# Kernel optimization log

Measured on AMD Instinct MI355X. Metric: run time of the kernel, lower is better.

Reference implementation:

```python
import jax, jax.numpy as jnp
import numpy as np

N = 50000   # nodes
E = 800000  # edges
C = 64      # node feature channels (0e)
A = 4       # edge attr channels
B = 16      # edge embedding (radial basis) size
H = 8       # radial MLP hidden size
D = 32      # query/key channels
P = 16      # node attr channels
R_MAX = 5.0


def setup_inputs() -> dict:
    key = jax.random.key(0)
    ks = jax.random.split(key, 20)
    w = lambda k, shape, fan_in: (jax.random.normal(k, shape, jnp.float32) / np.sqrt(fan_in).astype(np.float32))
    inp = {
        "node_feats": jax.random.normal(ks[0], (N, C), jnp.float32),
        "node_attrs": jax.random.normal(ks[1], (N, P), jnp.float32),
        "edge_embedding": jax.random.uniform(ks[2], (E, B), jnp.float32),
        "edge_attrs": jax.random.normal(ks[3], (E, A), jnp.float32),
        "positions": jax.random.normal(ks[4], (N, 3), jnp.float32) * 0.3,  # keep lengths < r_max
        "edge_src": jax.random.randint(ks[5], (E,), 0, N),
        "edge_dst": jax.random.randint(ks[6], (E,), 0, N),
        # parameters
        "W_q": w(ks[7], (C, D), C),            # h_q Linear
        "W1_k": w(ks[8], (B, H), B),           # radial MLP for tp_k
        "W2_k": w(ks[9], (H, C * A), H),
        "W1_v": w(ks[10], (B, H), B),          # radial MLP for tp_v
        "W2_v": w(ks[11], (H, C * A), H),
        "W_lin_k": w(ks[12], (C, D), C),       # linear_k
        "W_lin_v": w(ks[13], (C, C), C),       # linear_v
        "W_dot": w(ks[14], (D, D), D * D),     # FullyConnectedTensorProduct(q,k,'0e')
        "W_sc": w(ks[15], (C, P, C), C * P),   # self connection FCTP
    }
    return inp


def soft_unit_step(x):
    safe = jnp.where(x > 0, x, 1.0)
    return jnp.where(x > 0, jnp.exp(-1.0 / safe), 0.0)


def uvu_tp(x_src, edge_attrs, edge_embedding, W1, W2):
    # radial MLP -> per-edge, per-path weights [E, C, A]; 'uvu' tensor product on scalars
    wgt = (jax.nn.silu(edge_embedding @ W1) @ W2).reshape(-1, C, A)
    return x_src * (jnp.einsum('eca,ea->ec', wgt, edge_attrs) / np.sqrt(A).astype(np.float32))


def reference(node_feats, node_attrs, edge_embedding, edge_attrs, positions,
              edge_src, edge_dst, W_q, W1_k, W2_k, W1_v, W2_v,
              W_lin_k, W_lin_v, W_dot, W_sc):
    q = (node_feats @ W_q)[edge_dst]                              # [E, D]
    x_src = node_feats[edge_src]                                  # [E, C]
    k = uvu_tp(x_src, edge_attrs, edge_embedding, W1_k, W2_k) @ W_lin_k  # [E, D]
    v = uvu_tp(x_src, edge_attrs, edge_embedding, W1_v, W2_v) @ W_lin_v  # [E, C]

    edge_vec = positions[edge_dst] - positions[edge_src]
    edge_length = jnp.linalg.norm(edge_vec, axis=1)               # [E]
    cutoff = soft_unit_step(2.0 * R_MAX * (1.0 - edge_length / R_MAX))

    score = jnp.einsum('ei,ij,ej->e', q, W_dot, k)                # weighted bilinear dot -> 0e
    expv = cutoff * jnp.exp(score)                                # [E]
    z = jax.ops.segment_sum(expv, edge_dst, num_segments=N)       # softmax normalizer
    z = jnp.where(z == 0, 1.0, z)
    alpha = expv / z[edge_dst]
    msg = jnp.sqrt(jax.nn.relu(alpha))[:, None] * v               # [E, C]
    node_out = jax.ops.segment_sum(msg, edge_dst, num_segments=N)  # [N, C]

    sc = jnp.einsum('nc,np,cpo->no', node_feats, node_attrs, W_sc)
    return node_out + sc
```

## Files before the change

### kernel.cpp

```cpp
#include <hip/hip_runtime.h>
#include <math.h>

#define NN 50000
#define EE 800000
#define NPAD 50176
#define CPAD 68

typedef __attribute__((ext_vector_type(8))) short short8v;
typedef __attribute__((ext_vector_type(4))) float f32x4;

static __device__ __forceinline__ short bf16r(float x) {
  union { float f; unsigned u; } v; v.f = x;
  unsigned r = v.u + 0x7FFFu + ((v.u >> 16) & 1u);
  return (short)(r >> 16);
}
static __device__ __forceinline__ float bf2f(unsigned u) {
  union { unsigned u; float f; } v; v.u = u << 16;
  return v.f;
}
static __device__ __forceinline__ unsigned pk2(float a, float b) {
  return (unsigned)(unsigned short)bf16r(a) | ((unsigned)(unsigned short)bf16r(b) << 16);
}


__global__ __launch_bounds__(256) void fold_kernel(
    const float* __restrict__ Wq, const float* __restrict__ Wdot,
    const float* __restrict__ Wlk, const float* __restrict__ W2k,
    const float* __restrict__ W2v, const float* __restrict__ Wlv,
    float* __restrict__ M, unsigned short* __restrict__ w2kT,
    unsigned short* __restrict__ w2vT, unsigned short* __restrict__ wlvb)
{
  __shared__ float tmp[2048];
  const int tid = threadIdx.x;
#pragma unroll
  for (int r = 0; r < 8; ++r) {
    int idx = tid + r * 256;
    int cin = idx >> 5, d = idx & 31;
    float a = 0.f;
    for (int j = 0; j < 32; ++j) a = fmaf(Wq[cin * 32 + j], Wdot[j * 32 + d], a);
    tmp[idx] = a;
  }
  __syncthreads();
#pragma unroll
  for (int r = 0; r < 16; ++r) {
    int idx = tid + r * 256;
    int cin = idx >> 6, c = idx & 63;
    float a = 0.f;
    for (int d = 0; d < 32; ++d) a = fmaf(tmp[cin * 32 + d], Wlk[c * 32 + d], a);
    M[idx] = a;
  }
#pragma unroll
  for (int r = 0; r < 8; ++r) {
    int idx = tid + r * 256;
    int c = idx >> 5, k = idx & 31, h = k >> 2, a = k & 3;
    w2kT[idx] = (unsigned short)bf16r(W2k[h * 256 + c * 4 + a]);
    w2vT[idx] = (unsigned short)bf16r(W2v[h * 256 + c * 4 + a]);
  }
#pragma unroll
  for (int r = 0; r < 16; ++r) {
    int idx = tid + r * 256;
    int o = idx >> 6, c = idx & 63;
    wlvb[idx] = (unsigned short)bf16r(Wlv[c * 64 + o]);
  }
}

__global__ __launch_bounds__(256) void prep_wsc(
    const float* __restrict__ Wsc, unsigned short* __restrict__ wscb)
{
  int w = blockIdx.x * 256 + threadIdx.x;
  int c = w & 63, o = (w >> 6) & 63, p = w >> 12;
  wscb[w] = (unsigned short)bf16r(Wsc[c * 1024 + p * 64 + o]);
}

__global__ __launch_bounds__(256) void hist_kernel(
    const int* __restrict__ edst, int* __restrict__ cur)
{
  int e = blockIdx.x * 256 + threadIdx.x;
  atomicAdd(&cur[edst[e]], 1);
}

__global__ __launch_bounds__(256) void scanA_kernel(
    int* __restrict__ cur, int* __restrict__ bsum)
{
  __shared__ int s[256];
  const int tid = threadIdx.x;
  const int i = blockIdx.x * 256 + tid;
  int v = cur[i];
  s[tid] = v;
  __syncthreads();
  for (int off = 1; off < 256; off <<= 1) {
    int t = (tid >= off) ? s[tid - off] : 0;
    __syncthreads();
    s[tid] += t;
    __syncthreads();
  }
  cur[i] = s[tid] - v;
  if (tid == 255) bsum[blockIdx.x] = s[255];
}

__global__ __launch_bounds__(256) void scanB_kernel(int* __restrict__ bsum)
{
  __shared__ int s[256];
  const int tid = threadIdx.x;
  int v = (tid < 196) ? bsum[tid] : 0;
  s[tid] = v;
  __syncthreads();
  for (int off = 1; off < 256; off <<= 1) {
    int t = (tid >= off) ? s[tid - off] : 0;
    __syncthreads();
    s[tid] += t;
    __syncthreads();
  }
  if (tid < 196) bsum[tid] = s[tid] - v;
}

__global__ __launch_bounds__(256) void scanC_kernel(
    int* __restrict__ cur, const int* __restrict__ bsum)
{
  const int i = blockIdx.x * 256 + threadIdx.x;
  cur[i] += bsum[blockIdx.x];
}

__global__ __launch_bounds__(256) void scatter_fused(
    const int* __restrict__ esrc, const int* __restrict__ edst,
    const float* __restrict__ ea, const float* __restrict__ eb,
    const float* __restrict__ pos, const float* __restrict__ W1k,
    const float* __restrict__ W1v, int* __restrict__ cur,
    float* __restrict__ rec)
{
  int e = blockIdx.x * 256 + threadIdx.x;
  int s = esrc[e], d = edst[e];
  int r = atomicAdd(&cur[d], 1);
  float dx = pos[d * 3 + 0] - pos[s * 3 + 0];
  float dy = pos[d * 3 + 1] - pos[s * 3 + 1];
  float dz = pos[d * 3 + 2] - pos[s * 3 + 2];
  float len = sqrtf(fmaf(dx, dx, fmaf(dy, dy, dz * dz)));
  float arg = 10.f - 2.f * len;
  float cl = (arg > 0.f) ? __expf(-1.f / arg) : 0.f;
  const f32x4* eb4 = reinterpret_cast<const f32x4*>(eb);
  f32x4 q0 = eb4[e * 4 + 0], q1 = eb4[e * 4 + 1],
        q2 = eb4[e * 4 + 2], q3 = eb4[e * 4 + 3];
  float ebv[16] = {q0.x, q0.y, q0.z, q0.w, q1.x, q1.y, q1.z, q1.w,
                   q2.x, q2.y, q2.z, q2.w, q3.x, q3.y, q3.z, q3.w};
  float h[16];
#pragma unroll
  for (int j = 0; j < 16; ++j) h[j] = 0.f;
#pragma unroll
  for (int b = 0; b < 16; ++b) {
    float x = ebv[b];
#pragma unroll
    for (int j = 0; j < 8; ++j) {
      h[j]     = fmaf(x, W1k[b * 8 + j], h[j]);
      h[8 + j] = fmaf(x, W1v[b * 8 + j], h[8 + j]);
    }
  }
#pragma unroll
  for (int j = 0; j < 16; ++j) h[j] = h[j] / (1.f + __expf(-h[j]));

  f32x4* rp4 = reinterpret_cast<f32x4*>(rec + (size_t)r * 16);
  f32x4 w0, w1, w2, w3;
  w0.x = __int_as_float(s); w0.y = __int_as_float(d); w0.z = cl; w0.w = 0.f;
  w1 = reinterpret_cast<const f32x4*>(ea)[e];
  w2.x = __uint_as_float(pk2(h[0], h[1]));
  w2.y = __uint_as_float(pk2(h[2], h[3]));
  w2.z = __uint_as_float(pk2(h[4], h[5]));
  w2.w = __uint_as_float(pk2(h[6], h[7]));
  w3.x = __uint_as_float(pk2(h[8], h[9]));
  w3.y = __uint_as_float(pk2(h[10], h[11]));
  w3.z = __uint_as_float(pk2(h[12], h[13]));
  w3.w = __uint_as_float(pk2(h[14], h[15]));
  __builtin_nontemporal_store(w0, rp4 + 0);
  __builtin_nontemporal_store(w1, rp4 + 1);
  __builtin_nontemporal_store(w2, rp4 + 2);
  __builtin_nontemporal_store(w3, rp4 + 3);
}

__global__ __launch_bounds__(256) void tq_kernel(
    const float* __restrict__ nf, const float* __restrict__ M, float* __restrict__ tq)
{
  __shared__ float Ml[4096];
  __shared__ float nfl[64 * 68];
  const int tid = threadIdx.x;
  const int base = blockIdx.x * 64;
#pragma unroll
  for (int r = 0; r < 4; ++r) {
    int idx = tid + r * 256;
    reinterpret_cast<float4*>(Ml)[idx] = reinterpret_cast<const float4*>(M)[idx];
  }
#pragma unroll
  for (int r = 0; r < 4; ++r) {
    int idx = tid + r * 256;
    int row = idx >> 4, c4 = idx & 15;
    float4 v = make_float4(0.f, 0.f, 0.f, 0.f);
    if (base + row < NN) v = reinterpret_cast<const float4*>(nf)[(base + row) * 16 + c4];
    *reinterpret_cast<float4*>(&nfl[row * 68 + c4 * 4]) = v;
  }
  __syncthreads();
  const int to = tid & 15, tn = tid >> 4;
  float4 acc[4] = {make_float4(0,0,0,0), make_float4(0,0,0,0),
                   make_float4(0,0,0,0), make_float4(0,0,0,0)};
  for (int c = 0; c < 64; ++c) {
    float4 m = reinterpret_cast<const float4*>(Ml)[c * 16 + to];
#pragma unroll
    for (int i = 0; i < 4; ++i) {
      float x = nfl[(tn * 4 + i) * 68 + c];
      acc[i].x = fmaf(x, m.x, acc[i].x);
      acc[i].y = fmaf(x, m.y, acc[i].y);
      acc[i].z = fmaf(x, m.z, acc[i].z);
      acc[i].w = fmaf(x, m.w, acc[i].w);
    }
  }
#pragma unroll
  for (int i = 0; i < 4; ++i) {
    int n = base + tn * 4 + i;
    if (n < NN) reinterpret_cast<float4*>(tq)[n * 16 + to] = acc[i];
  }
}

__global__ __launch_bounds__(256) void edge_kernel(
    const float* __restrict__ nf, const float* __restrict__ tq,
    const float* __restrict__ rec,
    const unsigned short* __restrict__ w2kT, const unsigned short* __restrict__ w2vT,
    float* __restrict__ z, float* __restrict__ U)
{
  __shared__ float xs[64 * CPAD];
  __shared__ int   es[64];
  __shared__ int   ed[64];
  __shared__ float cl[64];
  __shared__ float evs[64];
  const int tid  = threadIdx.x;
  const int lane = tid & 63;
  const int lo = lane & 15, hi = lane >> 4;
  const int w = tid >> 6;
  const int sb = blockIdx.x * 64;
  const int row = 16 * w + lo;

  short8v bk[4], bv[4];
#pragma unroll
  for (int t = 0; t < 4; ++t) {
    bk[t] = *reinterpret_cast<const short8v*>(&w2kT[(16 * t + lo) * 32 + hi * 8]);
    bv[t] = *reinterpret_cast<const short8v*>(&w2vT[(16 * t + lo) * 32 + hi * 8]);
  }
  if (tid < 64) {
    float4 h0 = *reinterpret_cast<const float4*>(rec + (size_t)(sb + tid) * 16);
    es[tid] = __float_as_int(h0.x);
    ed[tid] = __float_as_int(h0.y);
    cl[tid] = h0.z;
  }
  const unsigned* ru = reinterpret_cast<const unsigned*>(rec);
  const size_t rb = (size_t)(sb + row) * 16;
  unsigned k01 = ru[rb + 8 + hi];
  unsigned v01 = ru[rb + 12 + hi];
  float4 a4 = *reinterpret_cast<const float4*>(rec + rb + 4);

  __syncthreads();

#pragma unroll
  for (int r = 0; r < 4; ++r) {
    int idx = tid + r * 256;
    int e = idx >> 4, c4 = idx & 15;
    float4 xv = reinterpret_cast<const float4*>(nf)[es[e] * 16 + c4];
    *reinterpret_cast<float4*>(&xs[e * CPAD + c4 * 4]) = xv;
  }

  float hk0 = bf2f(k01 & 0xffffu), hk1 = bf2f(k01 >> 16);
  float hv0 = bf2f(v01 & 0xffffu), hv1 = bf2f(v01 >> 16);
  short8v ak, av;
  ak[0] = bf16r(hk0 * a4.x); ak[1] = bf16r(hk0 * a4.y);
  ak[2] = bf16r(hk0 * a4.z); ak[3] = bf16r(hk0 * a4.w);
  ak[4] = bf16r(hk1 * a4.x); ak[5] = bf16r(hk1 * a4.y);
  ak[6] = bf16r(hk1 * a4.z); ak[7] = bf16r(hk1 * a4.w);
  av[0] = bf16r(hv0 * a4.x); av[1] = bf16r(hv0 * a4.y);
  av[2] = bf16r(hv0 * a4.z); av[3] = bf16r(hv0 * a4.w);
  av[4] = bf16r(hv1 * a4.x); av[5] = bf16r(hv1 * a4.y);
  av[6] = bf16r(hv1 * a4.z); av[7] = bf16r(hv1 * a4.w);

  __syncthreads();

  f32x4 zero = {0.f, 0.f, 0.f, 0.f};
  f32x4 ack[4], acv[4];
#pragma unroll
  for (int t = 0; t < 4; ++t) {
    ack[t] = __builtin_amdgcn_mfma_f32_16x16x32_bf16(ak, bk[t], zero, 0, 0, 0);
    acv[t] = __builtin_amdgcn_mfma_f32_16x16x32_bf16(av, bv[t], zero, 0, 0, 0);
  }

  const int erow = 16 * w + 4 * hi;
  float p0, p1, p2, p3;
  {
    const float* x0 = &xs[(erow + 0) * CPAD + lo];
    const float* x1 = &xs[(erow + 1) * CPAD + lo];
    const float* x2 = &xs[(erow + 2) * CPAD + lo];
    const float* x3 = &xs[(erow + 3) * CPAD + lo];
    const float* t0 = tq + (size_t)ed[erow + 0] * 64 + lo;
    const float* t1 = tq + (size_t)ed[erow + 1] * 64 + lo;
    const float* t2 = tq + (size_t)ed[erow + 2] * 64 + lo;
    const float* t3 = tq + (size_t)ed[erow + 3] * 64 + lo;
    p0 = (x0[0]*t0[0])*ack[0][0] + (x0[16]*t0[16])*ack[1][0] + (x0[32]*t0[32])*ack[2][0] + (x0[48]*t0[48])*ack[3][0];
    p1 = (x1[0]*t1[0])*ack[0][1] + (x1[16]*t1[16])*ack[1][1] + (x1[32]*t1[32])*ack[2][1] + (x1[48]*t1[48])*ack[3][1];
    p2 = (x2[0]*t2[0])*ack[0][2] + (x2[16]*t2[16])*ack[1][2] + (x2[32]*t2[32])*ack[2][2] + (x2[48]*t2[48])*ack[3][2];
    p3 = (x3[0]*t3[0])*ack[0][3] + (x3[16]*t3[16])*ack[1][3] + (x3[32]*t3[32])*ack[2][3] + (x3[48]*t3[48])*ack[3][3];
  }
#pragma unroll
  for (int off = 1; off < 16; off <<= 1) {
    p0 += __shfl_xor(p0, off);
    p1 += __shfl_xor(p1, off);
    p2 += __shfl_xor(p2, off);
    p3 += __shfl_xor(p3, off);
  }
  float ev0 = cl[erow + 0] * __expf(0.5f * p0);
  float ev1 = cl[erow + 1] * __expf(0.5f * p1);
  float ev2 = cl[erow + 2] * __expf(0.5f * p2);
  float ev3 = cl[erow + 3] * __expf(0.5f * p3);
  float se0 = sqrtf(ev0), se1 = sqrtf(ev1), se2 = sqrtf(ev2), se3 = sqrtf(ev3);
  if (lo < 4) {
    float ev = (lo == 0) ? ev0 : (lo == 1) ? ev1 : (lo == 2) ? ev2 : ev3;
    evs[erow + lo] = ev;
  }
#pragma unroll
  for (int i = 0; i < 4; ++i) {
    const float se = (i == 0) ? se0 : (i == 1) ? se1 : (i == 2) ? se2 : se3;
    float* xr = &xs[(erow + i) * CPAD + lo];
#pragma unroll
    for (int t = 0; t < 4; ++t) {
      xr[16 * t] = se * xr[16 * t] * acv[t][i];
    }
  }
  {
    const int c = lane;
    float acc = 0.f, evacc = 0.f;
    int prev = ed[16 * w];
    for (int r = 16 * w; r < 16 * w + 16; ++r) {
      int d = ed[r];
      if (d != prev) {
        unsafeAtomicAdd(&U[prev * 64 + c], acc);
        if (c == 0) unsafeAtomicAdd(&z[prev], evacc);
        acc = 0.f; evacc = 0.f; prev = d;
      }
      acc += xs[r * CPAD + c];
      if (c == 0) evacc += evs[r];
    }
    unsafeAtomicAdd(&U[prev * 64 + c], acc);
    if (c == 0) unsafeAtomicAdd(&z[prev], evacc);
  }
}

__global__ __launch_bounds__(256, 4) void final_kernel(
    const float* __restrict__ nf, const float* __restrict__ na,
    const float* __restrict__ U, const float* __restrict__ z,
    const unsigned short* __restrict__ wscb, const unsigned short* __restrict__ wlvb,
    float* __restrict__ out)
{
  __shared__ float nfl[64 * 68];
  __shared__ float Ul[64 * 68];
  __shared__ float nal[64 * 17];
  __shared__ float sl[64];
  const int tid = threadIdx.x;
  const int lane = tid & 63;
  const int lo = lane & 15, hi = lane >> 4;
  const int w = tid >> 6;
  const int nb = blockIdx.x * 64;

#pragma unroll
  for (int r = 0; r < 4; ++r) {
    int idx = tid + r * 256;
    int row = idx >> 4, c4 = idx & 15;
    int n = nb + row; if (n >= NN) n = NN - 1;
    float4 v = reinterpret_cast<const float4*>(nf)[n * 16 + c4];
    *reinterpret_cast<float4*>(&nfl[row * 68 + c4 * 4]) = v;
    float4 u = reinterpret_cast<const float4*>(U)[n * 16 + c4];
    *reinterpret_cast<float4*>(&Ul[row * 68 + c4 * 4]) = u;
  }
#pragma unroll
  for (int r = 0; r < 4; ++r) {
    int idx = tid + r * 256;
    int row = idx >> 4, p = idx & 15;
    int n = nb + row; if (n >= NN) n = NN - 1;
    nal[row * 17 + p] = na[n * 16 + p];
  }
  if (tid < 64) {
    int n = nb + tid; if (n >= NN) n = NN - 1;
    float zz = z[n];
    sl[tid] = (zz > 0.f) ? 0.5f * rsqrtf(zz) : 0.f;
  }
  __syncthreads();

  const int row = 16 * w + lo;
  short8v anf[2], au[2];
#pragma unroll
  for (int kk = 0; kk < 2; ++kk) {
#pragma unroll
    for (int j = 0; j < 8; ++j) {
      anf[kk][j] = bf16r(nfl[row * 68 + 32 * kk + 8 * hi + j]);
      au[kk][j]  = bf16r(Ul[row * 68 + 32 * kk + 8 * hi + j]);
    }
  }

  f32x4 zeroA = {0.f, 0.f, 0.f, 0.f};
  f32x4 accS[4] = {zeroA, zeroA, zeroA, zeroA};
  f32x4 accU[4] = {zeroA, zeroA, zeroA, zeroA};

#pragma unroll
  for (int t = 0; t < 4; ++t) {
    short8v b0 = *reinterpret_cast<const short8v*>(&wlvb[(16 * t + lo) * 64 + 8 * hi]);
    short8v b1 = *reinterpret_cast<const short8v*>(&wlvb[(16 * t + lo) * 64 + 32 + 8 * hi]);
    accU[t] = __builtin_amdgcn_mfma_f32_16x16x32_bf16(au[0], b0, accU[t], 0, 0, 0);
    accU[t] = __builtin_amdgcn_mfma_f32_16x16x32_bf16(au[1], b1, accU[t], 0, 0, 0);
  }
#pragma unroll 1
  for (int p = 0; p < 16; ++p) {
    f32x4 cp[4] = {zeroA, zeroA, zeroA, zeroA};
#pragma unroll
    for (int t = 0; t < 4; ++t) {
      const int bbase = (p * 64 + 16 * t + lo) * 64 + 8 * hi;
      short8v b0 = *reinterpret_cast<const short8v*>(&wscb[bbase]);
      short8v b1 = *reinterpret_cast<const short8v*>(&wscb[bbase + 32]);
      cp[t] = __builtin_amdgcn_mfma_f32_16x16x32_bf16(anf[0], b0, cp[t], 0, 0, 0);
      cp[t] = __builtin_amdgcn_mfma_f32_16x16x32_bf16(anf[1], b1, cp[t], 0, 0, 0);
    }
#pragma unroll
    for (int i = 0; i < 4; ++i) {
      float nav = nal[(16 * w + 4 * hi + i) * 17 + p];
#pragma unroll
      for (int t = 0; t < 4; ++t) accS[t][i] = fmaf(nav, cp[t][i], accS[t][i]);
    }
  }
#pragma unroll
  for (int i = 0; i < 4; ++i) {
    int n = nb + 16 * w + 4 * hi + i;
    if (n < NN) {
      float s = sl[16 * w + 4 * hi + i];
#pragma unroll
      for (int t = 0; t < 4; ++t) {
        out[n * 64 + 16 * t + lo] = fmaf(s, accU[t][i], accS[t][i]);
      }
    }
  }
}

extern "C" void kernel_launch(void* const* d_in, const int* in_sizes, int n_in,
                              void* d_out, int out_size, void* d_ws, size_t ws_size,
                              hipStream_t stream) {
  const float* nf   = (const float*)d_in[0];
  const float* na   = (const float*)d_in[1];
  const float* eb   = (const float*)d_in[2];
  const float* ea   = (const float*)d_in[3];
  const float* pos  = (const float*)d_in[4];
  const int*   esrc = (const int*)d_in[5];
  const int*   edst = (const int*)d_in[6];
  const float* Wq   = (const float*)d_in[7];
  const float* W1k  = (const float*)d_in[8];
  const float* W2k  = (const float*)d_in[9];
  const float* W1v  = (const float*)d_in[10];
  const float* W2v  = (const float*)d_in[11];
  const float* Wlk  = (const float*)d_in[12];
  const float* Wlv  = (const float*)d_in[13];
  const float* Wdot = (const float*)d_in[14];
  const float* Wsc  = (const float*)d_in[15];
  float* out = (float*)d_out;

  float* wsf = (float*)d_ws;
  float* z    = wsf;
  float* U    = wsf + 50176;
  int*   cur  = (int*)(wsf + 50176);
  int*   bsum = (int*)(wsf + 100352);
  float* M    = wsf + 100608;
  float* tq   = wsf + 3250176;
  unsigned short* wscb = (unsigned short*)(wsf + 3250176);
  unsigned short* w2kT = (unsigned short*)(wsf + 6450176);
  unsigned short* w2vT = (unsigned short*)(wsf + 6451200);
  unsigned short* wlvb = (unsigned short*)(wsf + 6452224);
  float* rec  = wsf + 6454272;

  fold_kernel<<<1, 256, 0, stream>>>(Wq, Wdot, Wlk, W2k, W2v, Wlv, M, w2kT, w2vT, wlvb);
  tq_kernel<<<(NN + 63) / 64, 256, 0, stream>>>(nf, M, tq);
  hipMemsetAsync(cur, 0, (size_t)(NPAD + 256) * sizeof(int), stream);
  hist_kernel<<<EE / 256, 256, 0, stream>>>(edst, cur);
  scanA_kernel<<<NPAD / 256, 256, 0, stream>>>(cur, bsum);
  scanB_kernel<<<1, 256, 0, stream>>>(bsum);
  scanC_kernel<<<NPAD / 256, 256, 0, stream>>>(cur, bsum);
  scatter_fused<<<EE / 256, 256, 0, stream>>>(esrc, edst, ea, eb, pos, W1k, W1v, cur, rec);
  hipMemsetAsync(z, 0, (size_t)3250176 * sizeof(float), stream);
  edge_kernel<<<EE / 64, 256, 0, stream>>>(nf, tq, rec, w2kT, w2vT, z, U);
  prep_wsc<<<256, 256, 0, stream>>>(Wsc, wscb);
  final_kernel<<<(NN + 63) / 64, 256, 0, stream>>>(nf, na, U, z, wscb, wlvb, out);
}
```

Measured before the change: 340.4 us.

## Write edge records in original order and gather via permutation index

The scatter kernel now writes a compact 48-byte record (cutoff, bf16 edge attrs, bf16 hidden) at the original edge index, coalesced, and records a permutation array mapping sorted position to edge. The edge kernel gathers src/dst from the input arrays and the record through the permutation. This trades random 64-byte scattered writes for random gathered reads in the edge kernel, and also quantizes edge attrs to bf16 to shrink the record.

```diff
diff --git a/kernel.cpp b/kernel.cpp
--- a/kernel.cpp
+++ b/kernel.cpp
@@ -126,11 +126,12 @@
     const float* __restrict__ ea, const float* __restrict__ eb,
     const float* __restrict__ pos, const float* __restrict__ W1k,
     const float* __restrict__ W1v, int* __restrict__ cur,
-    float* __restrict__ rec)
+    int* __restrict__ perm, float* __restrict__ rec)
 {
   int e = blockIdx.x * 256 + threadIdx.x;
   int s = esrc[e], d = edst[e];
   int r = atomicAdd(&cur[d], 1);
+  perm[r] = e;
   float dx = pos[d * 3 + 0] - pos[s * 3 + 0];
   float dy = pos[d * 3 + 1] - pos[s * 3 + 1];
   float dz = pos[d * 3 + 2] - pos[s * 3 + 2];
@@ -157,22 +158,24 @@
 #pragma unroll
   for (int j = 0; j < 16; ++j) h[j] = h[j] / (1.f + __expf(-h[j]));
 
-  f32x4* rp4 = reinterpret_cast<f32x4*>(rec + (size_t)r * 16);
-  f32x4 w0, w1, w2, w3;
-  w0.x = __int_as_float(s); w0.y = __int_as_float(d); w0.z = cl; w0.w = 0.f;
-  w1 = reinterpret_cast<const f32x4*>(ea)[e];
-  w2.x = __uint_as_float(pk2(h[0], h[1]));
-  w2.y = __uint_as_float(pk2(h[2], h[3]));
-  w2.z = __uint_as_float(pk2(h[4], h[5]));
-  w2.w = __uint_as_float(pk2(h[6], h[7]));
-  w3.x = __uint_as_float(pk2(h[8], h[9]));
-  w3.y = __uint_as_float(pk2(h[10], h[11]));
-  w3.z = __uint_as_float(pk2(h[12], h[13]));
-  w3.w = __uint_as_float(pk2(h[14], h[15]));
-  __builtin_nontemporal_store(w0, rp4 + 0);
-  __builtin_nontemporal_store(w1, rp4 + 1);
-  __builtin_nontemporal_store(w2, rp4 + 2);
-  __builtin_nontemporal_store(w3, rp4 + 3);
+  f32x4 a4 = reinterpret_cast<const f32x4*>(ea)[e];
+  f32x4* rp4 = reinterpret_cast<f32x4*>(rec + (size_t)e * 12);
+  f32x4 w0, w1, w2;
+  w0.x = cl;
+  w0.y = __uint_as_float(pk2(a4.x, a4.y));
+  w0.z = __uint_as_float(pk2(a4.z, a4.w));
+  w0.w = 0.f;
+  w1.x = __uint_as_float(pk2(h[0], h[1]));
+  w1.y = __uint_as_float(pk2(h[2], h[3]));
+  w1.z = __uint_as_float(pk2(h[4], h[5]));
+  w1.w = __uint_as_float(pk2(h[6], h[7]));
+  w2.x = __uint_as_float(pk2(h[8], h[9]));
+  w2.y = __uint_as_float(pk2(h[10], h[11]));
+  w2.z = __uint_as_float(pk2(h[12], h[13]));
+  w2.w = __uint_as_float(pk2(h[14], h[15]));
+  rp4[0] = w0;
+  rp4[1] = w1;
+  rp4[2] = w2;
 }
 
 __global__ __launch_bounds__(256) void tq_kernel(
@@ -219,7 +222,8 @@
 
 __global__ __launch_bounds__(256) void edge_kernel(
     const float* __restrict__ nf, const float* __restrict__ tq,
-    const float* __restrict__ rec,
+    const float* __restrict__ rec, const int* __restrict__ perm,
+    const int* __restrict__ esrc, const int* __restrict__ edst,
     const unsigned short* __restrict__ w2kT, const unsigned short* __restrict__ w2vT,
     float* __restrict__ z, float* __restrict__ U)
 {
@@ -241,17 +245,19 @@
     bk[t] = *reinterpret_cast<const short8v*>(&w2kT[(16 * t + lo) * 32 + hi * 8]);
     bv[t] = *reinterpret_cast<const short8v*>(&w2vT[(16 * t + lo) * 32 + hi * 8]);
   }
+  const int eL = perm[sb + row];
   if (tid < 64) {
-    float4 h0 = *reinterpret_cast<const float4*>(rec + (size_t)(sb + tid) * 16);
-    es[tid] = __float_as_int(h0.x);
-    ed[tid] = __float_as_int(h0.y);
-    cl[tid] = h0.z;
+    int pe = perm[sb + tid];
+    es[tid] = esrc[pe];
+    ed[tid] = edst[pe];
+    cl[tid] = rec[(size_t)pe * 12];
   }
   const unsigned* ru = reinterpret_cast<const unsigned*>(rec);
-  const size_t rb = (size_t)(sb + row) * 16;
-  unsigned k01 = ru[rb + 8 + hi];
-  unsigned v01 = ru[rb + 12 + hi];
-  float4 a4 = *reinterpret_cast<const float4*>(rec + rb + 4);
+  const size_t rb = (size_t)eL * 12;
+  unsigned ea01 = ru[rb + 1];
+  unsigned ea23 = ru[rb + 2];
+  unsigned k01 = ru[rb + 4 + hi];
+  unsigned v01 = ru[rb + 8 + hi];
 
   __syncthreads();
 
@@ -263,17 +269,19 @@
     *reinterpret_cast<float4*>(&xs[e * CPAD + c4 * 4]) = xv;
   }
 
+  float ax = bf2f(ea01 & 0xffffu), ay = bf2f(ea01 >> 16);
+  float az = bf2f(ea23 & 0xffffu), aw = bf2f(ea23 >> 16);
   float hk0 = bf2f(k01 & 0xffffu), hk1 = bf2f(k01 >> 16);
   float hv0 = bf2f(v01 & 0xffffu), hv1 = bf2f(v01 >> 16);
   short8v ak, av;
-  ak[0] = bf16r(hk0 * a4.x); ak[1] = bf16r(hk0 * a4.y);
-  ak[2] = bf16r(hk0 * a4.z); ak[3] = bf16r(hk0 * a4.w);
-  ak[4] = bf16r(hk1 * a4.x); ak[5] = bf16r(hk1 * a4.y);
-  ak[6] = bf16r(hk1 * a4.z); ak[7] = bf16r(hk1 * a4.w);
-  av[0] = bf16r(hv0 * a4.x); av[1] = bf16r(hv0 * a4.y);
-  av[2] = bf16r(hv0 * a4.z); av[3] = bf16r(hv0 * a4.w);
-  av[4] = bf16r(hv1 * a4.x); av[5] = bf16r(hv1 * a4.y);
-  av[6] = bf16r(hv1 * a4.z); av[7] = bf16r(hv1 * a4.w);
+  ak[0] = bf16r(hk0 * ax); ak[1] = bf16r(hk0 * ay);
+  ak[2] = bf16r(hk0 * az); ak[3] = bf16r(hk0 * aw);
+  ak[4] = bf16r(hk1 * ax); ak[5] = bf16r(hk1 * ay);
+  ak[6] = bf16r(hk1 * az); ak[7] = bf16r(hk1 * aw);
+  av[0] = bf16r(hv0 * ax); av[1] = bf16r(hv0 * ay);
+  av[2] = bf16r(hv0 * az); av[3] = bf16r(hv0 * aw);
+  av[4] = bf16r(hv1 * ax); av[5] = bf16r(hv1 * ay);
+  av[6] = bf16r(hv1 * az); av[7] = bf16r(hv1 * aw);
 
   __syncthreads();
 
@@ -471,6 +479,7 @@
   unsigned short* w2vT = (unsigned short*)(wsf + 6451200);
   unsigned short* wlvb = (unsigned short*)(wsf + 6452224);
   float* rec  = wsf + 6454272;
+  int*   perm = (int*)(wsf + 16054272);
 
   fold_kernel<<<1, 256, 0, stream>>>(Wq, Wdot, Wlk, W2k, W2v, Wlv, M, w2kT, w2vT, wlvb);
   tq_kernel<<<(NN + 63) / 64, 256, 0, stream>>>(nf, M, tq);
@@ -479,9 +488,11 @@
   scanA_kernel<<<NPAD / 256, 256, 0, stream>>>(cur, bsum);
   scanB_kernel<<<1, 256, 0, stream>>>(bsum);
   scanC_kernel<<<NPAD / 256, 256, 0, stream>>>(cur, bsum);
-  scatter_fused<<<EE / 256, 256, 0, stream>>>(esrc, edst, ea, eb, pos, W1k, W1v, cur, rec);
+  scatter_fused<<<EE / 256, 256, 0, stream>>>(esrc, edst, ea, eb, pos, W1k, W1v,
+                                              cur, perm, rec);
   hipMemsetAsync(z, 0, (size_t)3250176 * sizeof(float), stream);
-  edge_kernel<<<EE / 64, 256, 0, stream>>>(nf, tq, rec, w2kT, w2vT, z, U);
+  edge_kernel<<<EE / 64, 256, 0, stream>>>(nf, tq, rec, perm, esrc, edst,
+                                           w2kT, w2vT, z, U);
   prep_wsc<<<256, 256, 0, stream>>>(Wsc, wscb);
   final_kernel<<<(NN + 63) / 64, 256, 0, stream>>>(nf, na, U, z, wscb, wlvb, out);
 }
```

New measurement: 322.7 us. 5.2% less time.
